# Kernel optimization log

Hardware: AMD Instinct MI355X
Metric: run time of the kernel (lower is better)

## Reference

```python
import jax, jax.numpy as jnp
import numpy as np
import math

C_ATOM = 128
C_PAIR = 16
N_HEADS = 4
C_HEAD = C_ATOM // N_HEADS
N_ATOMS = 2048

def _layer_norm(x, w, b, eps=1e-5):
    mu = jnp.mean(x, axis=-1, keepdims=True)
    var = jnp.var(x, axis=-1, keepdims=True)
    return (x - mu) * jax.lax.rsqrt(var + eps) * w + b

def setup_inputs() -> dict:
    key = jax.random.key(0)
    ks = jax.random.split(key, 20)
    s = 0.02
    return {
        "ql": jax.random.normal(ks[0], (N_ATOMS, C_ATOM), jnp.float32),
        "cl": jax.random.normal(ks[1], (N_ATOMS, C_ATOM), jnp.float32),
        "plm": jax.random.normal(ks[2], (N_ATOMS, N_ATOMS, C_PAIR), jnp.float32),
        "beta_mask": jax.random.normal(ks[3], (N_ATOMS, N_ATOMS), jnp.float32),
        "norm_q_w": jnp.ones((C_ATOM,), jnp.float32),
        "norm_q_b": jnp.zeros((C_ATOM,), jnp.float32),
        "norm_pair_w": jnp.ones((C_PAIR,), jnp.float32),
        "norm_pair_b": jnp.zeros((C_PAIR,), jnp.float32),
        "Wq": jax.random.normal(ks[4], (C_ATOM, C_ATOM), jnp.float32) * s,
        "bq": jnp.zeros((C_ATOM,), jnp.float32),
        "Wk": jax.random.normal(ks[5], (C_ATOM, C_ATOM), jnp.float32) * s,
        "Wv": jax.random.normal(ks[6], (C_ATOM, C_ATOM), jnp.float32) * s,
        "Wpb": jax.random.normal(ks[7], (N_HEADS, C_PAIR), jnp.float32) * s,
        "Wg": jax.random.normal(ks[8], (C_ATOM, C_ATOM), jnp.float32) * s,
        "Wo": jax.random.normal(ks[9], (C_ATOM, C_ATOM), jnp.float32) * s,
        "t_ln_w": jnp.ones((C_ATOM,), jnp.float32),
        "t_ln_b": jnp.zeros((C_ATOM,), jnp.float32),
        "W1": jax.random.normal(ks[10], (4 * C_ATOM, C_ATOM), jnp.float32) * s,
        "b1": jnp.zeros((4 * C_ATOM,), jnp.float32),
        "W2": jax.random.normal(ks[11], (C_ATOM, 4 * C_ATOM), jnp.float32) * s,
        "b2": jnp.zeros((C_ATOM,), jnp.float32),
    }

def reference(ql, cl, plm, beta_mask, norm_q_w, norm_q_b, norm_pair_w, norm_pair_b,
              Wq, bq, Wk, Wv, Wpb, Wg, Wo, t_ln_w, t_ln_b, W1, b1, W2, b2):
    n = ql.shape[0]
    ql_norm = _layer_norm(ql, norm_q_w, norm_q_b)  # [N, C]
    q = (ql_norm @ Wq.T + bq).reshape(n, N_HEADS, C_HEAD)
    k = (ql_norm @ Wk.T).reshape(n, N_HEADS, C_HEAD)
    v = (ql_norm @ Wv.T).reshape(n, N_HEADS, C_HEAD)
    # pair-biased logits: [H, N, N]
    logits = jnp.einsum('ihc,jhc->hij', q, k) / math.sqrt(C_HEAD)
    pair_bias = _layer_norm(plm, norm_pair_w, norm_pair_b) @ Wpb.T  # [N, N, H]
    logits = logits + jnp.transpose(pair_bias, (2, 0, 1)) + beta_mask[None]
    attn = jax.nn.softmax(logits, axis=-1)
    attn_out = jnp.einsum('hij,jhc->ihc', attn, v).reshape(n, C_ATOM)
    gate = jax.nn.sigmoid(ql_norm @ Wg.T)
    out = (gate * attn_out) @ Wo.T
    ql = ql + out
    # transition MLP
    t = _layer_norm(ql, t_ln_w, t_ln_b)
    ql = ql + jax.nn.relu(t @ W1.T + b1) @ W2.T + b2
    return ql
```

## Files before the change

kernel.cpp:

```cpp
#include <hip/hip_runtime.h>
#include <hip/hip_bf16.h>
#include <math.h>

#define NA 2048
#define CP 16

__global__ __launch_bounds__(256) void bias_kernel(
    const float* __restrict__ plm, const float* __restrict__ beta_mask,
    const float* __restrict__ npw, const float* __restrict__ npb,
    const float* __restrict__ Wpb,
    __hip_bfloat16* __restrict__ biasT)
{
    const int t = threadIdx.x;
    const int quad = t & 3;
    const int jloc = t >> 2;
    const int jc = blockIdx.x & 31;
    const int ic = blockIdx.x >> 5;
    const int j = jc * 64 + jloc;
    const int i0 = ic * 8;

    float w0[4], w1[4], w2[4], w3[4];
    {
        const float4 a = *(const float4*)(Wpb + 0 * 16 + quad * 4);
        w0[0] = a.x; w0[1] = a.y; w0[2] = a.z; w0[3] = a.w;
        const float4 b = *(const float4*)(Wpb + 1 * 16 + quad * 4);
        w1[0] = b.x; w1[1] = b.y; w1[2] = b.z; w1[3] = b.w;
        const float4 c = *(const float4*)(Wpb + 2 * 16 + quad * 4);
        w2[0] = c.x; w2[1] = c.y; w2[2] = c.z; w2[3] = c.w;
        const float4 d = *(const float4*)(Wpb + 3 * 16 + quad * 4);
        w3[0] = d.x; w3[1] = d.y; w3[2] = d.z; w3[3] = d.w;
    }
    const float4 nw = *(const float4*)(npw + quad * 4);
    const float4 nb = *(const float4*)(npb + quad * 4);

#pragma unroll
    for (int ii = 0; ii < 8; ++ii) {
        const int i = i0 + ii;
        const float4 x = *(const float4*)(plm + ((size_t)i * NA + j) * CP + quad * 4);
        float s = x.x + x.y + x.z + x.w;
        float s2 = x.x * x.x + x.y * x.y + x.z * x.z + x.w * x.w;
        s += __shfl_xor(s, 1); s2 += __shfl_xor(s2, 1);
        s += __shfl_xor(s, 2); s2 += __shfl_xor(s2, 2);
        const float mu = s * 0.0625f;
        const float inv = rsqrtf(s2 * 0.0625f - mu * mu + 1e-5f);
        const float x0 = (x.x - mu) * inv * nw.x + nb.x;
        const float x1 = (x.y - mu) * inv * nw.y + nb.y;
        const float x2 = (x.z - mu) * inv * nw.z + nb.z;
        const float x3 = (x.w - mu) * inv * nw.w + nb.w;
        float p0 = x0 * w0[0] + x1 * w0[1] + x2 * w0[2] + x3 * w0[3];
        float p1 = x0 * w1[0] + x1 * w1[1] + x2 * w1[2] + x3 * w1[3];
        float p2 = x0 * w2[0] + x1 * w2[1] + x2 * w2[2] + x3 * w2[3];
        float p3 = x0 * w3[0] + x1 * w3[1] + x2 * w3[2] + x3 * w3[3];
        p0 += __shfl_xor(p0, 1); p1 += __shfl_xor(p1, 1);
        p2 += __shfl_xor(p2, 1); p3 += __shfl_xor(p3, 1);
        p0 += __shfl_xor(p0, 2); p1 += __shfl_xor(p1, 2);
        p2 += __shfl_xor(p2, 2); p3 += __shfl_xor(p3, 2);
        const float bm = beta_mask[(size_t)i * NA + j];
        const float sel = (quad == 0) ? p0 : (quad == 1) ? p1 : (quad == 2) ? p2 : p3;
        biasT[(size_t)quad * NA * NA + (size_t)i * NA + j] = __float2bfloat16(sel + bm);
    }
}

__global__ __launch_bounds__(256) void qkvg_kernel(
    const float* __restrict__ ql,
    const float* __restrict__ nqw, const float* __restrict__ nqb,
    const float* __restrict__ Wq, const float* __restrict__ bq,
    const float* __restrict__ Wk, const float* __restrict__ Wv,
    const float* __restrict__ Wg,
    float* __restrict__ q_out, float* __restrict__ kT_out,
    float* __restrict__ vT_out, float* __restrict__ g_out)
{
    __shared__ float x_lds[4 * 128];
    __shared__ float xn_lds[4 * 128];
    const int t = threadIdx.x;
    const int row0 = blockIdx.x * 4;

    for (int idx = t; idx < 512; idx += 256)
        x_lds[idx] = ql[(size_t)row0 * 128 + idx];
    __syncthreads();

    if (t < 128) {
        const int r = t >> 5, id = t & 31;
        const float4 x4 = ((const float4*)x_lds)[r * 32 + id];
        float s = x4.x + x4.y + x4.z + x4.w;
        float s2 = x4.x * x4.x + x4.y * x4.y + x4.z * x4.z + x4.w * x4.w;
#pragma unroll
        for (int m = 16; m >= 1; m >>= 1) {
            s += __shfl_xor(s, m);
            s2 += __shfl_xor(s2, m);
        }
        const float mu = s * (1.0f / 128.0f);
        const float inv = rsqrtf(s2 * (1.0f / 128.0f) - mu * mu + 1e-5f);
#pragma unroll
        for (int k = 0; k < 4; ++k) {
            const int c = id * 4 + k;
            xn_lds[r * 128 + c] = (x_lds[r * 128 + c] - mu) * inv * nqw[c] + nqb[c];
        }
    }
    __syncthreads();

    const float4* xn4 = (const float4*)xn_lds;
#pragma unroll
    for (int cc = 0; cc < 2; ++cc) {
        const int col = cc * 256 + t;
        const int m = col >> 7;
        const int cl = col & 127;
        const float* W = (m == 0) ? Wq : (m == 1) ? Wk : (m == 2) ? Wv : Wg;
        float acc[4] = {0, 0, 0, 0};
        const float4* wrow = (const float4*)(W + (size_t)cl * 128);
#pragma unroll 8
        for (int k4 = 0; k4 < 32; ++k4) {
            const float4 w4 = wrow[k4];
#pragma unroll
            for (int r = 0; r < 4; ++r) {
                const float4 a = xn4[r * 32 + k4];
                acc[r] += a.x * w4.x + a.y * w4.y + a.z * w4.z + a.w * w4.w;
            }
        }
        if (m == 0) {
            const float bb = bq[cl];
            const float sc = 0.17677669529663687f;
#pragma unroll
            for (int r = 0; r < 4; ++r)
                q_out[(size_t)(row0 + r) * 128 + cl] = (acc[r] + bb) * sc;
        } else if (m == 1) {
            float4 o; o.x = acc[0]; o.y = acc[1]; o.z = acc[2]; o.w = acc[3];
            *(float4*)(kT_out + (size_t)cl * NA + row0) = o;
        } else if (m == 2) {
            float4 o; o.x = acc[0]; o.y = acc[1]; o.z = acc[2]; o.w = acc[3];
            *(float4*)(vT_out + (size_t)cl * NA + row0) = o;
        } else {
#pragma unroll
            for (int r = 0; r < 4; ++r)
                g_out[(size_t)(row0 + r) * 128 + cl] = 1.0f / (1.0f + __expf(-acc[r]));
        }
    }
}

__global__ __launch_bounds__(256) void attn_kernel(
    const __hip_bfloat16* __restrict__ biasT,
    const float* __restrict__ q_ws, const float* __restrict__ kT,
    const float* __restrict__ vT, const float* __restrict__ g_ws,
    float* __restrict__ attn_g)
{
    __shared__ unsigned short Lp[8][2048];
    __shared__ float q_s[8 * 32];
    __shared__ float redA[4 * 8];
    __shared__ float redB[4 * 8];
    __shared__ float opart[4 * 8 * 32];

    const int t = threadIdx.x;
    const int h = blockIdx.x & 3;
    const int i0 = (blockIdx.x >> 2) * 8;
    const int w = t >> 6, lane = t & 63;
    const int jq = w * 512;

    q_s[t] = q_ws[(size_t)(i0 + (t >> 5)) * 128 + h * 32 + (t & 31)];
    __syncthreads();

    float4 La[8], Lb[8];
#pragma unroll
    for (int r = 0; r < 8; ++r) {
        const __hip_bfloat16* base = biasT + (size_t)h * NA * NA + (size_t)(i0 + r) * NA;
        const __hip_bfloat162* ba = (const __hip_bfloat162*)(base + jq + lane * 4);
        const float2 f0 = __bfloat1622float2(ba[0]);
        const float2 f1 = __bfloat1622float2(ba[1]);
        La[r] = make_float4(f0.x, f0.y, f1.x, f1.y);
        const __hip_bfloat162* bb = (const __hip_bfloat162*)(base + jq + 256 + lane * 4);
        const float2 g0 = __bfloat1622float2(bb[0]);
        const float2 g1 = __bfloat1622float2(bb[1]);
        Lb[r] = make_float4(g0.x, g0.y, g1.x, g1.y);
    }

    const float* kb = kT + (size_t)(h * 32) * NA + jq + lane * 4;
#pragma unroll 4
    for (int c = 0; c < 32; ++c) {
        const float4 ka = *(const float4*)(kb + (size_t)c * NA);
        const float4 kc = *(const float4*)(kb + (size_t)c * NA + 256);
#pragma unroll
        for (int r = 0; r < 8; ++r) {
            const float qv = q_s[r * 32 + c];
            La[r].x += qv * ka.x; La[r].y += qv * ka.y;
            La[r].z += qv * ka.z; La[r].w += qv * ka.w;
            Lb[r].x += qv * kc.x; Lb[r].y += qv * kc.y;
            Lb[r].z += qv * kc.z; Lb[r].w += qv * kc.w;
        }
    }

#pragma unroll
    for (int r = 0; r < 8; ++r) {
        float m = fmaxf(fmaxf(fmaxf(La[r].x, La[r].y), fmaxf(La[r].z, La[r].w)),
                        fmaxf(fmaxf(Lb[r].x, Lb[r].y), fmaxf(Lb[r].z, Lb[r].w)));
#pragma unroll
        for (int mk = 32; mk >= 1; mk >>= 1) m = fmaxf(m, __shfl_xor(m, mk));
        if (lane == 0) redA[w * 8 + r] = m;
    }
    __syncthreads();
#pragma unroll
    for (int r = 0; r < 8; ++r) {
        const float m = fmaxf(fmaxf(redA[r], redA[8 + r]), fmaxf(redA[16 + r], redA[24 + r]));
        La[r].x = __expf(La[r].x - m); La[r].y = __expf(La[r].y - m);
        La[r].z = __expf(La[r].z - m); La[r].w = __expf(La[r].w - m);
        Lb[r].x = __expf(Lb[r].x - m); Lb[r].y = __expf(Lb[r].y - m);
        Lb[r].z = __expf(Lb[r].z - m); Lb[r].w = __expf(Lb[r].w - m);
        float s = La[r].x + La[r].y + La[r].z + La[r].w +
                  Lb[r].x + Lb[r].y + Lb[r].z + Lb[r].w;
#pragma unroll
        for (int mk = 32; mk >= 1; mk >>= 1) s += __shfl_xor(s, mk);
        if (lane == 0) redB[w * 8 + r] = s;
    }
    __syncthreads();
#pragma unroll
    for (int r = 0; r < 8; ++r) {
        const float invl = 1.0f / (redB[r] + redB[8 + r] + redB[16 + r] + redB[24 + r]);
        __hip_bfloat162* d = (__hip_bfloat162*)&Lp[r][jq + lane * 4];
        d[0] = __float22bfloat162_rn(make_float2(La[r].x * invl, La[r].y * invl));
        d[1] = __float22bfloat162_rn(make_float2(La[r].z * invl, La[r].w * invl));
        __hip_bfloat162* d2 = (__hip_bfloat162*)&Lp[r][jq + 256 + lane * 4];
        d2[0] = __float22bfloat162_rn(make_float2(Lb[r].x * invl, Lb[r].y * invl));
        d2[1] = __float22bfloat162_rn(make_float2(Lb[r].z * invl, Lb[r].w * invl));
    }
    __syncthreads();

    const int c = lane & 31, jh = lane >> 5;
    const int jb = jq + jh * 256;
    const float* vbase = vT + (size_t)(h * 32 + c) * NA + jb;
    float o[8] = {0, 0, 0, 0, 0, 0, 0, 0};
#pragma unroll 4
    for (int jf = 0; jf < 64; ++jf) {
        const float4 v4 = *(const float4*)(vbase + jf * 4);
#pragma unroll
        for (int r = 0; r < 8; ++r) {
            const __hip_bfloat162* pp = (const __hip_bfloat162*)&Lp[r][jb + jf * 4];
            const float2 pa = __bfloat1622float2(pp[0]);
            const float2 pb = __bfloat1622float2(pp[1]);
            o[r] += pa.x * v4.x + pa.y * v4.y + pb.x * v4.z + pb.y * v4.w;
        }
    }
#pragma unroll
    for (int r = 0; r < 8; ++r) {
        o[r] += __shfl_xor(o[r], 32);
        if (lane < 32) opart[w * 256 + r * 32 + c] = o[r];
    }
    __syncthreads();
    {
        const int r = t >> 5, cc = t & 31;
        const float val = opart[r * 32 + cc] + opart[256 + r * 32 + cc] +
                          opart[512 + r * 32 + cc] + opart[768 + r * 32 + cc];
        const float g = g_ws[(size_t)(i0 + r) * 128 + h * 32 + cc];
        attn_g[(size_t)(i0 + r) * 128 + h * 32 + cc] = val * g;
    }
}

__global__ __launch_bounds__(256) void out_mlp_kernel(
    const float* __restrict__ ql,
    const float* __restrict__ attn_g,
    const float* __restrict__ Wo,
    const float* __restrict__ tlw, const float* __restrict__ tlb,
    const float* __restrict__ W1, const float* __restrict__ b1,
    const float* __restrict__ W2, const float* __restrict__ b2,
    float* __restrict__ out)
{
    __shared__ float a_lds[4 * 128];
    __shared__ float ql2_lds[4 * 128];
    __shared__ float t_lds[4 * 128];
    __shared__ float h1_lds[4 * 512];
    const int t = threadIdx.x;
    const int row0 = blockIdx.x * 4;

    for (int idx = t; idx < 512; idx += 256)
        a_lds[idx] = attn_g[(size_t)row0 * 128 + idx];
    __syncthreads();

    {
        const int col = t >> 1, kh = t & 1;
        float p[4] = {0, 0, 0, 0};
        const float4* wr = (const float4*)(Wo + (size_t)col * 128 + kh * 64);
        const float4* a4 = (const float4*)a_lds;
#pragma unroll 8
        for (int k4 = 0; k4 < 16; ++k4) {
            const float4 w4 = wr[k4];
#pragma unroll
            for (int r = 0; r < 4; ++r) {
                const float4 a = a4[r * 32 + kh * 16 + k4];
                p[r] += a.x * w4.x + a.y * w4.y + a.z * w4.z + a.w * w4.w;
            }
        }
#pragma unroll
        for (int r = 0; r < 4; ++r) p[r] += __shfl_xor(p[r], 1);
        if (kh == 0) {
#pragma unroll
            for (int r = 0; r < 4; ++r)
                ql2_lds[r * 128 + col] = ql[(size_t)(row0 + r) * 128 + col] + p[r];
        }
    }
    __syncthreads();

    if (t < 128) {
        const int r = t >> 5, id = t & 31;
        const float4 x4 = ((const float4*)ql2_lds)[r * 32 + id];
        float s = x4.x + x4.y + x4.z + x4.w;
        float s2 = x4.x * x4.x + x4.y * x4.y + x4.z * x4.z + x4.w * x4.w;
#pragma unroll
        for (int m = 16; m >= 1; m >>= 1) {
            s += __shfl_xor(s, m);
            s2 += __shfl_xor(s2, m);
        }
        const float mu = s * (1.0f / 128.0f);
        const float inv = rsqrtf(s2 * (1.0f / 128.0f) - mu * mu + 1e-5f);
#pragma unroll
        for (int k = 0; k < 4; ++k) {
            const int c = id * 4 + k;
            t_lds[r * 128 + c] = (ql2_lds[r * 128 + c] - mu) * inv * tlw[c] + tlb[c];
        }
    }
    __syncthreads();

    const float4* t4 = (const float4*)t_lds;
#pragma unroll
    for (int cc = 0; cc < 2; ++cc) {
        const int col = cc * 256 + t;
        float acc[4] = {0, 0, 0, 0};
        const float4* wr = (const float4*)(W1 + (size_t)col * 128);
#pragma unroll 8
        for (int k4 = 0; k4 < 32; ++k4) {
            const float4 w4 = wr[k4];
#pragma unroll
            for (int r = 0; r < 4; ++r) {
                const float4 a = t4[r * 32 + k4];
                acc[r] += a.x * w4.x + a.y * w4.y + a.z * w4.z + a.w * w4.w;
            }
        }
        const float bb = b1[col];
#pragma unroll
        for (int r = 0; r < 4; ++r)
            h1_lds[r * 512 + col] = fmaxf(acc[r] + bb, 0.0f);
    }
    __syncthreads();

    {
        const int col = t >> 1, kh = t & 1;
        float p[4] = {0, 0, 0, 0};
        const float4* wr = (const float4*)(W2 + (size_t)col * 512 + kh * 256);
        const float4* h4 = (const float4*)h1_lds;
#pragma unroll 8
        for (int k4 = 0; k4 < 64; ++k4) {
            const float4 w4 = wr[k4];
#pragma unroll
            for (int r = 0; r < 4; ++r) {
                const float4 a = h4[r * 128 + kh * 64 + k4];
                p[r] += a.x * w4.x + a.y * w4.y + a.z * w4.z + a.w * w4.w;
            }
        }
#pragma unroll
        for (int r = 0; r < 4; ++r) p[r] += __shfl_xor(p[r], 1);
        if (kh == 0) {
            const float bb = b2[col];
#pragma unroll
            for (int r = 0; r < 4; ++r)
                out[(size_t)(row0 + r) * 128 + col] = ql2_lds[r * 128 + col] + p[r] + bb;
        }
    }
}

extern "C" void kernel_launch(void* const* d_in, const int* in_sizes, int n_in,
                              void* d_out, int out_size, void* d_ws, size_t ws_size,
                              hipStream_t stream) {
    const float* ql   = (const float*)d_in[0];
    const float* plm  = (const float*)d_in[2];
    const float* beta = (const float*)d_in[3];
    const float* nqw  = (const float*)d_in[4];
    const float* nqb  = (const float*)d_in[5];
    const float* npw  = (const float*)d_in[6];
    const float* npb  = (const float*)d_in[7];
    const float* Wq   = (const float*)d_in[8];
    const float* bq   = (const float*)d_in[9];
    const float* Wk   = (const float*)d_in[10];
    const float* Wv   = (const float*)d_in[11];
    const float* Wpb  = (const float*)d_in[12];
    const float* Wg   = (const float*)d_in[13];
    const float* Wo   = (const float*)d_in[14];
    const float* tlw  = (const float*)d_in[15];
    const float* tlb  = (const float*)d_in[16];
    const float* W1   = (const float*)d_in[17];
    const float* b1   = (const float*)d_in[18];
    const float* W2   = (const float*)d_in[19];
    const float* b2   = (const float*)d_in[20];
    float* out = (float*)d_out;

    char* ws = (char*)d_ws;
    __hip_bfloat16* biasT = (__hip_bfloat16*)ws;
    float* q_ws  = (float*)(ws + 33554432);
    float* g_ws  = (float*)(ws + 33554432 + 1 * 1048576);
    float* kT_ws = (float*)(ws + 33554432 + 2 * 1048576);
    float* vT_ws = (float*)(ws + 33554432 + 3 * 1048576);
    float* ag_ws = (float*)(ws + 33554432 + 4 * 1048576);

    bias_kernel<<<8192, 256, 0, stream>>>(plm, beta, npw, npb, Wpb, biasT);
    qkvg_kernel<<<NA / 4, 256, 0, stream>>>(ql, nqw, nqb, Wq, bq, Wk, Wv, Wg,
                                            q_ws, kT_ws, vT_ws, g_ws);
    attn_kernel<<<NA / 2, 256, 0, stream>>>(biasT, q_ws, kT_ws, vT_ws, g_ws, ag_ws);
    out_mlp_kernel<<<NA / 4, 256, 0, stream>>>(ql, ag_ws, Wo, tlw, tlb,
                                               W1, b1, W2, b2, out);
}
```

Baseline: 532.9 us.

## Restructure P·V loop so each wave owns 8 channels across all keys

The attention-times-V stage now assigns each wave 8 output channels over the full key range, with lanes splitting keys. Each thread loads its softmax probabilities once and reuses them across 8 channels, instead of re-reading LDS probabilities for every channel. The partial sums are reduced with cross-lane shuffles and a small LDS pass that reuses the probability buffer. This raises register use to 64 accumulators per thread, which may reduce occupancy, and adds shuffle reduction work.

```diff
diff --git a/kernel.cpp b/kernel.cpp
--- a/kernel.cpp
+++ b/kernel.cpp
@@ -147,7 +147,6 @@
     __shared__ float q_s[8 * 32];
     __shared__ float redA[4 * 8];
     __shared__ float redB[4 * 8];
-    __shared__ float opart[4 * 8 * 32];
 
     const int t = threadIdx.x;
     const int h = blockIdx.x & 3;
@@ -222,33 +221,64 @@
     }
     __syncthreads();
 
-    const int c = lane & 31, jh = lane >> 5;
-    const int jb = jq + jh * 256;
-    const float* vbase = vT + (size_t)(h * 32 + c) * NA + jb;
-    float o[8] = {0, 0, 0, 0, 0, 0, 0, 0};
-#pragma unroll 4
-    for (int jf = 0; jf < 64; ++jf) {
-        const float4 v4 = *(const float4*)(vbase + jf * 4);
+    float o[8][8];
+#pragma unroll
+    for (int r = 0; r < 8; ++r)
+#pragma unroll
+        for (int cc = 0; cc < 8; ++cc) o[r][cc] = 0.0f;
+
+    const float* vb0 = vT + (size_t)(h * 32 + w * 8) * NA;
+#pragma unroll 2
+    for (int jf = 0; jf < 8; ++jf) {
+        const int joff = jf * 256 + lane * 4;
+        float2 pa[8], pb[8];
 #pragma unroll
         for (int r = 0; r < 8; ++r) {
-            const __hip_bfloat162* pp = (const __hip_bfloat162*)&Lp[r][jb + jf * 4];
-            const float2 pa = __bfloat1622float2(pp[0]);
-            const float2 pb = __bfloat1622float2(pp[1]);
-            o[r] += pa.x * v4.x + pa.y * v4.y + pb.x * v4.z + pb.y * v4.w;
-        }
-    }
+            const __hip_bfloat162* pp = (const __hip_bfloat162*)&Lp[r][joff];
+            pa[r] = __bfloat1622float2(pp[0]);
+            pb[r] = __bfloat1622float2(pp[1]);
+        }
+#pragma unroll
+        for (int cc = 0; cc < 8; ++cc) {
+            const float4 v4 = *(const float4*)(vb0 + (size_t)cc * NA + joff);
+#pragma unroll
+            for (int r = 0; r < 8; ++r) {
+                o[r][cc] += pa[r].x * v4.x + pa[r].y * v4.y +
+                            pb[r].x * v4.z + pb[r].y * v4.w;
+            }
+        }
+    }
+
+    __syncthreads();
+    float* op = (float*)&Lp[0][0];
 #pragma unroll
     for (int r = 0; r < 8; ++r) {
-        o[r] += __shfl_xor(o[r], 32);
-        if (lane < 32) opart[w * 256 + r * 32 + c] = o[r];
-    }
-    __syncthreads();
+#pragma unroll
+        for (int cc = 0; cc < 8; ++cc) {
+            float s = o[r][cc];
+            s += __shfl_xor(s, 32);
+            s += __shfl_xor(s, 16);
+            s += __shfl_xor(s, 8);
+            o[r][cc] = s;
+        }
+    }
+    if (lane < 8) {
+#pragma unroll
+        for (int r = 0; r < 8; ++r)
+#pragma unroll
+            for (int cc = 0; cc < 8; ++cc)
+                op[((w * 8 + r) * 8 + cc) * 8 + lane] = o[r][cc];
+    }
+    __syncthreads();
+
     {
-        const int r = t >> 5, cc = t & 31;
-        const float val = opart[r * 32 + cc] + opart[256 + r * 32 + cc] +
-                          opart[512 + r * 32 + cc] + opart[768 + r * 32 + cc];
-        const float g = g_ws[(size_t)(i0 + r) * 128 + h * 32 + cc];
-        attn_g[(size_t)(i0 + r) * 128 + h * 32 + cc] = val * g;
+        const float4 a = ((const float4*)op)[t * 2];
+        const float4 b = ((const float4*)op)[t * 2 + 1];
+        const float s = a.x + a.y + a.z + a.w + b.x + b.y + b.z + b.w;
+        const int r = (t >> 3) & 7;
+        const int c = (t >> 6) * 8 + (t & 7);
+        const float g = g_ws[(size_t)(i0 + r) * 128 + h * 32 + c];
+        attn_g[(size_t)(i0 + r) * 128 + h * 32 + c] = s * g;
     }
 }
 
```

Measured after the change: 531.3 us. Within noise of the previous version (-0.3%).
